# Performance work log

Measured on AMD Instinct MI355X. Metric: run time of the kernel, lower is better.

## Reference

```python
import jax, jax.numpy as jnp
import numpy as np

N = 50000
E = 800000
IN, H, OUT = 128, 96, 64
BN_EPS = 1e-5


def setup_inputs() -> dict:
    key = jax.random.key(0)
    ks = jax.random.split(key, 16)
    x = jax.random.normal(ks[0], (N, IN), dtype=jnp.float32)
    edge_index = jax.random.randint(ks[1], (2, E), 0, N, dtype=jnp.int64)
    edge_weight = jax.random.uniform(ks[2], (E,), dtype=jnp.float32)
    def lin(k, fo, fi):
        # PyG glorot-ish init
        s = 1.0 / np.sqrt(fi)
        return jax.random.uniform(k, (fo, fi), minval=-s, maxval=s, dtype=jnp.float32)
    W1, b1 = lin(ks[3], H, IN), jnp.zeros((H,), jnp.float32)
    W2, b2 = lin(ks[4], H, H), jnp.zeros((H,), jnp.float32)
    W3, b3 = lin(ks[5], OUT, H), jnp.zeros((OUT,), jnp.float32)
    g1 = jnp.ones((H,), jnp.float32); beta1 = jnp.zeros((H,), jnp.float32)
    m1 = 0.1 * jax.random.normal(ks[6], (H,), dtype=jnp.float32)
    v1 = jnp.abs(1.0 + 0.1 * jax.random.normal(ks[7], (H,), dtype=jnp.float32))
    g2 = jnp.ones((H,), jnp.float32); beta2 = jnp.zeros((H,), jnp.float32)
    m2 = 0.1 * jax.random.normal(ks[8], (H,), dtype=jnp.float32)
    v2 = jnp.abs(1.0 + 0.1 * jax.random.normal(ks[9], (H,), dtype=jnp.float32))
    return dict(x=x, edge_index=edge_index, edge_weight=edge_weight,
                W1=W1, b1=b1, W2=W2, b2=b2, W3=W3, b3=b3,
                g1=g1, beta1=beta1, m1=m1, v1=v1,
                g2=g2, beta2=beta2, m2=m2, v2=v2)


def gcn_norm(edge_index, edge_weight, n):
    # PyG gcn_norm with add_self_loops=True, fill_value=1.0
    loop = jnp.arange(n, dtype=edge_index.dtype)
    row = jnp.concatenate([edge_index[0], loop])  # sources
    col = jnp.concatenate([edge_index[1], loop])  # targets
    ew = jnp.concatenate([edge_weight, jnp.ones((n,), edge_weight.dtype)])
    deg = jax.ops.segment_sum(ew, col, num_segments=n)
    dis = jnp.where(deg > 0, jax.lax.rsqrt(deg), 0.0)  # inf -> 0 masked_fill
    norm = dis[row] * ew * dis[col]
    return row, col, norm


def gcn_conv(x, row, col, norm, W, b, n):
    xw = x @ W.T                       # [N, F_out] dense transform first
    msg = norm[:, None] * xw[row]      # [E+N, F_out] gather + edge scale
    out = jax.ops.segment_sum(msg, col, num_segments=n)  # scatter-add
    return out + b


def bn_eval(x, gamma, beta, mean, var):
    return (x - mean) * jax.lax.rsqrt(var + BN_EPS) * gamma + beta


def reference(x, edge_index, edge_weight, W1, b1, W2, b2, W3, b3,
              g1, beta1, m1, v1, g2, beta2, m2, v2):
    n = x.shape[0]
    row, col, norm = gcn_norm(edge_index, edge_weight, n)  # cached=True: shared
    h = gcn_conv(x, row, col, norm, W1, b1, n)
    h = jax.nn.relu(bn_eval(h, g1, beta1, m1, v1))
    h = gcn_conv(h, row, col, norm, W2, b2, n)
    h = jax.nn.relu(bn_eval(h, g2, beta2, m2, v2))
    out = gcn_conv(h, row, col, norm, W3, b3, n)
    return out
```

## Files before the change

### kernel.cpp

```cpp
#include <hip/hip_runtime.h>
#include <hip/hip_fp16.h>


constexpr float BN_EPS = 1e-5f;
constexpr float FIXED_SCALE = 33554432.0f;
constexpr float INV_FIXED_SCALE = 1.0f / 33554432.0f;
constexpr float NORM_SCALE = 32768.0f;
constexpr float INV_NORM_SCALE = 1.0f / 32768.0f;

typedef _Float16 f16x8 __attribute__((ext_vector_type(8)));
typedef float f32x4 __attribute__((ext_vector_type(4)));


template <int K, int F, bool F32X, bool F32W>
__device__ __forceinline__ void gemm_block(const void* __restrict__ Xin,
                                           const void* __restrict__ Win,
                                           _Float16* __restrict__ Y,
                                           int n0b, int tid, int n,
                                           _Float16* lds) {
    constexpr int KT = K / 32;
    constexpr int FT = F / 16;
    constexpr int LROW = (F == 96) ? 104 : 72;
    int wave = tid >> 6;
    int lane = tid & 63;
    int quad = lane >> 4;
    int r = lane & 15;
    int n0 = n0b + wave * 16;
    bool active = (n0 < n);

    if (active) {
        f16x8 a[KT];
        if (F32X) {
            const float* xr = (const float*)Xin + (size_t)(n0 + r) * K + quad * 8;
#pragma unroll
            for (int kt = 0; kt < KT; ++kt) {
                float4 v0 = *(const float4*)(xr + kt * 32);
                float4 v1 = *(const float4*)(xr + kt * 32 + 4);
                f16x8 t = {(_Float16)v0.x, (_Float16)v0.y, (_Float16)v0.z, (_Float16)v0.w,
                           (_Float16)v1.x, (_Float16)v1.y, (_Float16)v1.z, (_Float16)v1.w};
                a[kt] = t;
            }
        } else {
            const f16x8* xr = (const f16x8*)((const _Float16*)Xin + (size_t)(n0 + r) * K + quad * 8);
#pragma unroll
            for (int kt = 0; kt < KT; ++kt) a[kt] = xr[kt * 4];
        }

        f32x4 acc[FT];
#pragma unroll
        for (int ft = 0; ft < FT; ++ft) acc[ft] = (f32x4){0.f, 0.f, 0.f, 0.f};

#pragma unroll
        for (int kt = 0; kt < KT; ++kt) {
#pragma unroll
            for (int ft = 0; ft < FT; ++ft) {
                f16x8 b;
                if (F32W) {
                    const float* wr = (const float*)Win + (size_t)(ft * 16 + r) * K + kt * 32 + quad * 8;
                    float4 v0 = *(const float4*)wr;
                    float4 v1 = *(const float4*)(wr + 4);
                    f16x8 t = {(_Float16)v0.x, (_Float16)v0.y, (_Float16)v0.z, (_Float16)v0.w,
                               (_Float16)v1.x, (_Float16)v1.y, (_Float16)v1.z, (_Float16)v1.w};
                    b = t;
                } else {
                    b = *(const f16x8*)((const _Float16*)Win + (size_t)(ft * 16 + r) * K + kt * 32 + quad * 8);
                }
                acc[ft] = __builtin_amdgcn_mfma_f32_16x16x32_f16(a[kt], b, acc[ft], 0, 0, 0);
            }
        }

#pragma unroll
        for (int ft = 0; ft < FT; ++ft) {
#pragma unroll
            for (int reg = 0; reg < 4; ++reg) {
                int lr = wave * 16 + quad * 4 + reg;
                lds[(size_t)lr * LROW + ft * 16 + r] = (_Float16)acc[ft][reg];
            }
        }
    }
    __syncthreads();

    constexpr int CPR = F / 8;
    constexpr int TOTAL = 64 * CPR;
    for (int i = tid; i < TOTAL; i += 256) {
        int row = i / CPR, c = i - row * CPR;
        int grow = n0b + row;
        if (grow < n)
            *(uint4*)(Y + (size_t)grow * F + c * 8) =
                *(const uint4*)(lds + (size_t)row * LROW + c * 8);
    }
}

template <int K, int F>
__global__ __launch_bounds__(256) void k_gemm(const _Float16* __restrict__ X,
                                              const _Float16* __restrict__ Wh,
                                              _Float16* __restrict__ Y, int n) {
    __shared__ _Float16 lds[64 * 104];
    gemm_block<K, F, false, false>(X, Wh, Y, blockIdx.x * 64, threadIdx.x, n, lds);
}


__global__ __launch_bounds__(256) void k_mega(
    const int* __restrict__ col_idx, const float* __restrict__ ew,
    unsigned long long* packed, int* rank, int e_cnt, int pair_b,
    const float* __restrict__ x, const float* __restrict__ W1,
    _Float16* __restrict__ bufA, int n,
    const float* __restrict__ W2, const float* __restrict__ W3,
    _Float16* __restrict__ w2h, _Float16* __restrict__ w3h,
    int w2n4, int w3n4) {
    __shared__ _Float16 lds[64 * 104];
    int b = blockIdx.x;
    if (b < 2 * pair_b) {
        int q = b >> 1;
        if ((b & 1) == 0) {
#pragma unroll
            for (int j = 0; j < 4; ++j) {
                int e = q * 1024 + j * 256 + (int)threadIdx.x;
                if (e < e_cnt) {
                    int c = col_idx[e];
                    unsigned wfix = (unsigned)(ew[e] * FIXED_SCALE + 0.5f);
                    unsigned long long inc = (1ull << 32) | (unsigned long long)wfix;
                    unsigned long long old = atomicAdd(&packed[c], inc);
                    rank[e] = (int)(old >> 32);
                }
            }
        } else {
            gemm_block<128, 96, true, true>(x, W1, bufA, q * 64, threadIdx.x, n, lds);
        }
    } else {
        int i = (b - 2 * pair_b) * 256 + (int)threadIdx.x;
        const float* src; _Float16* dst; int o;
        if (i < w2n4) { src = W2; dst = w2h; o = i; }
        else if (i < w2n4 + w3n4) { src = W3; dst = w3h; o = i - w2n4; }
        else return;
        float4 v = ((const float4*)src)[o];
        __half2 h0 = __floats2half2_rn(v.x, v.y);
        __half2 h1 = __floats2half2_rn(v.z, v.w);
        *(uint2*)(dst + (size_t)o * 4) = make_uint2(*(unsigned*)&h0, *(unsigned*)&h1);
    }
}


__global__ void k_scan1(const unsigned long long* __restrict__ packed,
                        int* bsum, float* dis, int n) {
    __shared__ int s[256];
    int i = blockIdx.x * 256 + threadIdx.x;
    int cnt = 0;
    if (i < n) {
        unsigned long long p = packed[i];
        cnt = (int)(p >> 32);
        float wsum = (float)(unsigned)(p & 0xffffffffull) * INV_FIXED_SCALE;
        dis[i] = rsqrtf(1.0f + wsum);
    }
    s[threadIdx.x] = cnt;
    __syncthreads();
    for (int off = 128; off > 0; off >>= 1) {
        if ((int)threadIdx.x < off) s[threadIdx.x] += s[threadIdx.x + off];
        __syncthreads();
    }
    if (threadIdx.x == 0) bsum[blockIdx.x] = s[0];
}

__global__ void k_scan23(const unsigned long long* __restrict__ packed,
                         const int* __restrict__ bsum,
                         int* row_ptr, int n, int e_total, int nb) {
    __shared__ int sb[256];
    __shared__ int s[256];
    int t = threadIdx.x;
    int bv = (t < nb) ? bsum[t] : 0;
    sb[t] = bv;
    __syncthreads();
    for (int off = 1; off < 256; off <<= 1) {
        int x = (t >= off) ? sb[t - off] : 0;
        __syncthreads();
        sb[t] += x;
        __syncthreads();
    }
    int boff = (blockIdx.x == 0) ? 0 : sb[blockIdx.x - 1];

    int i = blockIdx.x * 256 + t;
    int v = (i < n) ? (int)(packed[i] >> 32) : 0;
    s[t] = v;
    __syncthreads();
    for (int off = 1; off < 256; off <<= 1) {
        int x = (t >= off) ? s[t - off] : 0;
        __syncthreads();
        s[t] += x;
        __syncthreads();
    }
    int ex = s[t] - v + boff;
    if (i < n) row_ptr[i] = ex;
    if (i == 0) row_ptr[n] = e_total;
}

__global__ void k_fill(const int* __restrict__ row_idx, const int* __restrict__ col_idx,
                       const float* __restrict__ ew, const float* __restrict__ dis,
                       const int* __restrict__ row_ptr, const int* __restrict__ rank,
                       unsigned* ep, int e_cnt) {
    int e = blockIdx.x * 256 + threadIdx.x;
    if (e < e_cnt) {
        int r = row_idx[e];
        int c = col_idx[e];
        float nm = dis[r] * ew[e] * dis[c];
        unsigned q = (unsigned)(nm * NORM_SCALE + 0.5f);
        if (q > 65535u) q = 65535u;
        ep[row_ptr[c] + rank[e]] = ((unsigned)r << 16) | q;
    }
}


__device__ inline void cvt8(uint4 u, float* f) {
    float2 t;
    t = __half22float2(*(const __half2*)&u.x); f[0] = t.x; f[1] = t.y;
    t = __half22float2(*(const __half2*)&u.y); f[2] = t.x; f[3] = t.y;
    t = __half22float2(*(const __half2*)&u.z); f[4] = t.x; f[5] = t.y;
    t = __half22float2(*(const __half2*)&u.w); f[6] = t.x; f[7] = t.y;
}

__device__ inline void h8_acc(uint4 u, float w, float acc[8]) {
    float2 a = __half22float2(*(const __half2*)&u.x);
    float2 b = __half22float2(*(const __half2*)&u.y);
    float2 c = __half22float2(*(const __half2*)&u.z);
    float2 d = __half22float2(*(const __half2*)&u.w);
    acc[0] = fmaf(w, a.x, acc[0]); acc[1] = fmaf(w, a.y, acc[1]);
    acc[2] = fmaf(w, b.x, acc[2]); acc[3] = fmaf(w, b.y, acc[3]);
    acc[4] = fmaf(w, c.x, acc[4]); acc[5] = fmaf(w, c.y, acc[5]);
    acc[6] = fmaf(w, d.x, acc[6]); acc[7] = fmaf(w, d.y, acc[7]);
}

template <int F, bool BN, bool F32OUT>
__global__ __launch_bounds__(256) void k_aggr(
    const _Float16* __restrict__ xw, const int* __restrict__ row_ptr,
    const unsigned* __restrict__ ep,
    const float* __restrict__ dis, const float* __restrict__ bias,
    const float* __restrict__ g, const float* __restrict__ beta,
    const float* __restrict__ m, const float* __restrict__ v,
    void* __restrict__ out, int n) {
    constexpr int FQ = F / 8;
    int tg = blockIdx.x * 256 + threadIdx.x;
    int node = tg / FQ;
    int q = tg - node * FQ;
    if (node >= n) return;

    const uint4* __restrict__ base = (const uint4*)xw;

    float acc[8];
    {
        float d = dis[node];
        float d2 = d * d;
        uint4 sv = base[(size_t)node * FQ + q];
        float t[8];
        cvt8(sv, t);
#pragma unroll
        for (int j = 0; j < 8; ++j) acc[j] = d2 * t[j];
    }

    int e0 = row_ptr[node], e1 = row_ptr[node + 1];
    int e = e0;
    for (; e + 4 <= e1; e += 4) {
        unsigned p0 = ep[e + 0], p1 = ep[e + 1], p2 = ep[e + 2], p3 = ep[e + 3];
        uint4 x0 = base[(size_t)(p0 >> 16) * FQ + q];
        uint4 x1 = base[(size_t)(p1 >> 16) * FQ + q];
        uint4 x2 = base[(size_t)(p2 >> 16) * FQ + q];
        uint4 x3 = base[(size_t)(p3 >> 16) * FQ + q];
        h8_acc(x0, (float)(p0 & 0xffffu) * INV_NORM_SCALE, acc);
        h8_acc(x1, (float)(p1 & 0xffffu) * INV_NORM_SCALE, acc);
        h8_acc(x2, (float)(p2 & 0xffffu) * INV_NORM_SCALE, acc);
        h8_acc(x3, (float)(p3 & 0xffffu) * INV_NORM_SCALE, acc);
    }
    for (; e < e1; ++e) {
        unsigned p = ep[e];
        uint4 xv = base[(size_t)(p >> 16) * FQ + q];
        h8_acc(xv, (float)(p & 0xffffu) * INV_NORM_SCALE, acc);
    }

    int fb = q * 8;
    const float4* bb = (const float4*)(bias + fb);
    float4 b0 = bb[0], b1 = bb[1];
    acc[0] += b0.x; acc[1] += b0.y; acc[2] += b0.z; acc[3] += b0.w;
    acc[4] += b1.x; acc[5] += b1.y; acc[6] += b1.z; acc[7] += b1.w;
    if (BN) {
#pragma unroll
        for (int j = 0; j < 8; ++j) {
            acc[j] = fmaxf((acc[j] - m[fb + j]) * rsqrtf(v[fb + j] + BN_EPS) * g[fb + j]
                           + beta[fb + j], 0.f);
        }
    }
    if (F32OUT) {
        float* op = (float*)out + (size_t)node * F + fb;
        *(float4*)(op + 0) = make_float4(acc[0], acc[1], acc[2], acc[3]);
        *(float4*)(op + 4) = make_float4(acc[4], acc[5], acc[6], acc[7]);
    } else {
        __half2 h0 = __floats2half2_rn(acc[0], acc[1]);
        __half2 h1 = __floats2half2_rn(acc[2], acc[3]);
        __half2 h2 = __floats2half2_rn(acc[4], acc[5]);
        __half2 h3 = __floats2half2_rn(acc[6], acc[7]);
        uint4 u = make_uint4(*(unsigned*)&h0, *(unsigned*)&h1,
                             *(unsigned*)&h2, *(unsigned*)&h3);
        ((uint4*)out)[(size_t)node * FQ + q] = u;
    }
}


extern "C" void kernel_launch(void* const* d_in, const int* in_sizes, int n_in,
                              void* d_out, int out_size, void* d_ws, size_t ws_size,
                              hipStream_t stream) {
    constexpr int IN = 128, H = 96, OUT = 64;

    const float* x   = (const float*)d_in[0];
    const int*   ei  = (const int*)d_in[1];
    const float* ew  = (const float*)d_in[2];
    const float* W1  = (const float*)d_in[3];
    const float* b1  = (const float*)d_in[4];
    const float* W2  = (const float*)d_in[5];
    const float* b2  = (const float*)d_in[6];
    const float* W3  = (const float*)d_in[7];
    const float* b3  = (const float*)d_in[8];
    const float* g1  = (const float*)d_in[9];
    const float* be1 = (const float*)d_in[10];
    const float* m1  = (const float*)d_in[11];
    const float* v1  = (const float*)d_in[12];
    const float* g2  = (const float*)d_in[13];
    const float* be2 = (const float*)d_in[14];
    const float* m2  = (const float*)d_in[15];
    const float* v2  = (const float*)d_in[16];

    const int N = in_sizes[0] / IN;
    const int E = in_sizes[2];
    const int* row_idx = ei;
    const int* col_idx = ei + E;

    char* ws = (char*)d_ws;
    size_t off = 0;
    auto alloc = [&](size_t bytes) -> void* {
        void* p = ws + off;
        off = (off + bytes + 255) & ~(size_t)255;
        return p;
    };
    unsigned long long* packed = (unsigned long long*)alloc((size_t)N * 8);
    float*     dis     = (float*)alloc((size_t)N * 4);
    int*       row_ptr = (int*)alloc((size_t)(N + 1) * 4);
    int*       bsum    = (int*)alloc(256 * 4);
    int*       rank    = (int*)alloc((size_t)E * 4);
    unsigned*  ep      = (unsigned*)alloc((size_t)E * 4);
    _Float16*  w2h     = (_Float16*)alloc((size_t)H * H * 2);
    _Float16*  w3h     = (_Float16*)alloc((size_t)OUT * H * 2);
    _Float16*  bufA    = (_Float16*)alloc((size_t)N * H * 2);
    _Float16*  bufB    = (_Float16*)alloc((size_t)N * H * 2);
    (void)ws_size; (void)n_in; (void)out_size;

    constexpr int W2N4 = H * H / 4, W3N4 = OUT * H / 4;
    const int NB = (N + 255) / 256;
    const int DEG1024 = (E + 1023) / 1024;
    const int GG = (N / 16 + 3) / 4;
    const int PAIR = (DEG1024 > GG) ? DEG1024 : GG;
    const int CVT_B = (W2N4 + W3N4 + 255) / 256;

    hipMemsetAsync(packed, 0, (size_t)N * 8, stream);
    k_mega<<<2 * PAIR + CVT_B, 256, 0, stream>>>(
        col_idx, ew, packed, rank, E, PAIR,
        x, W1, bufA, N, W2, W3, w2h, w3h, W2N4, W3N4);
    k_scan1<<<NB, 256, 0, stream>>>(packed, bsum, dis, N);
    k_scan23<<<NB, 256, 0, stream>>>(packed, bsum, row_ptr, N, E, NB);
    k_fill<<<(E + 255) / 256, 256, 0, stream>>>(row_idx, col_idx, ew, dis,
                                                row_ptr, rank, ep, E);

    const int GA96 = ((size_t)N * (H / 8) + 255) / 256;
    const int GA64 = ((size_t)N * (OUT / 8) + 255) / 256;

    k_aggr<H, true, false><<<GA96, 256, 0, stream>>>(
        bufA, row_ptr, ep, dis, b1, g1, be1, m1, v1, bufB, N);

    k_gemm<H, H><<<GG, 256, 0, stream>>>(bufB, w2h, bufA, N);
    k_aggr<H, true, false><<<GA96, 256, 0, stream>>>(
        bufA, row_ptr, ep, dis, b2, g2, be2, m2, v2, bufB, N);

    k_gemm<H, OUT><<<GG, 256, 0, stream>>>(bufB, w3h, bufA, N);
    k_aggr<OUT, false, true><<<GA64, 256, 0, stream>>>(
        bufA, row_ptr, ep, dis, b3, nullptr, nullptr, nullptr, nullptr, d_out, N);
}
```

Before: 264.9 us.

## Store GEMM outputs feature-sliced and map aggregation slices to XCDs for L2 locality

The GEMM epilogue now writes its output as separate feature slices: four slices of 24 halfs for width 96, two slices of 32 for width 64. The aggregation kernel picks its slice from the low bits of blockIdx. Because blocks are dispatched round-robin across XCDs, each XCD should mostly gather from one smaller slice that fits its L2, rather than from the whole feature matrix. The cost is narrower 48-byte gather segments per row and a dependence on the hardware's block-to-XCD scheduling order.

```diff
diff --git a/kernel.cpp b/kernel.cpp
--- a/kernel.cpp
+++ b/kernel.cpp
@@ -21,6 +21,8 @@
     constexpr int KT = K / 32;
     constexpr int FT = F / 16;
     constexpr int LROW = (F == 96) ? 104 : 72;
+    constexpr int CPS = (F == 96) ? 3 : 4;
+    constexpr int SHW = (F == 96) ? 24 : 32;
     int wave = tid >> 6;
     int lane = tid & 63;
     int quad = lane >> 4;
@@ -84,9 +86,10 @@
     constexpr int TOTAL = 64 * CPR;
     for (int i = tid; i < TOTAL; i += 256) {
         int row = i / CPR, c = i - row * CPR;
+        int s = c / CPS, off = c - s * CPS;
         int grow = n0b + row;
         if (grow < n)
-            *(uint4*)(Y + (size_t)grow * F + c * 8) =
+            *(uint4*)(Y + ((size_t)s * n + grow) * SHW + off * 8) =
                 *(const uint4*)(lds + (size_t)row * LROW + c * 8);
     }
 }
@@ -236,19 +239,23 @@
     const float* __restrict__ g, const float* __restrict__ beta,
     const float* __restrict__ m, const float* __restrict__ v,
     void* __restrict__ out, int n) {
-    constexpr int FQ = F / 8;
-    int tg = blockIdx.x * 256 + threadIdx.x;
-    int node = tg / FQ;
-    int q = tg - node * FQ;
+    constexpr int S   = (F == 96) ? 4 : 2;
+    constexpr int CPS = (F == 96) ? 3 : 4;
+    constexpr int SHW = (F == 96) ? 24 : 32;
+    constexpr int SH  = (F == 96) ? 2 : 1;
+    int sb = blockIdx.x & (S - 1);
+    int idx = ((int)blockIdx.x >> SH) * 256 + (int)threadIdx.x;
+    int node = idx / CPS;
+    int c = idx - node * CPS;
     if (node >= n) return;
 
-    const uint4* __restrict__ base = (const uint4*)xw;
+    const uint4* __restrict__ base = (const uint4*)(xw + (size_t)sb * n * SHW);
 
     float acc[8];
     {
         float d = dis[node];
         float d2 = d * d;
-        uint4 sv = base[(size_t)node * FQ + q];
+        uint4 sv = base[(size_t)node * CPS + c];
         float t[8];
         cvt8(sv, t);
 #pragma unroll
@@ -259,10 +266,10 @@
     int e = e0;
     for (; e + 4 <= e1; e += 4) {
         unsigned p0 = ep[e + 0], p1 = ep[e + 1], p2 = ep[e + 2], p3 = ep[e + 3];
-        uint4 x0 = base[(size_t)(p0 >> 16) * FQ + q];
-        uint4 x1 = base[(size_t)(p1 >> 16) * FQ + q];
-        uint4 x2 = base[(size_t)(p2 >> 16) * FQ + q];
-        uint4 x3 = base[(size_t)(p3 >> 16) * FQ + q];
+        uint4 x0 = base[(size_t)(p0 >> 16) * CPS + c];
+        uint4 x1 = base[(size_t)(p1 >> 16) * CPS + c];
+        uint4 x2 = base[(size_t)(p2 >> 16) * CPS + c];
+        uint4 x3 = base[(size_t)(p3 >> 16) * CPS + c];
         h8_acc(x0, (float)(p0 & 0xffffu) * INV_NORM_SCALE, acc);
         h8_acc(x1, (float)(p1 & 0xffffu) * INV_NORM_SCALE, acc);
         h8_acc(x2, (float)(p2 & 0xffffu) * INV_NORM_SCALE, acc);
@@ -270,11 +277,11 @@
     }
     for (; e < e1; ++e) {
         unsigned p = ep[e];
-        uint4 xv = base[(size_t)(p >> 16) * FQ + q];
+        uint4 xv = base[(size_t)(p >> 16) * CPS + c];
         h8_acc(xv, (float)(p & 0xffffu) * INV_NORM_SCALE, acc);
     }
 
-    int fb = q * 8;
+    int fb = sb * SHW + c * 8;
     const float4* bb = (const float4*)(bias + fb);
     float4 b0 = bb[0], b1 = bb[1];
     acc[0] += b0.x; acc[1] += b0.y; acc[2] += b0.z; acc[3] += b0.w;
@@ -297,7 +304,7 @@
         __half2 h3 = __floats2half2_rn(acc[6], acc[7]);
         uint4 u = make_uint4(*(unsigned*)&h0, *(unsigned*)&h1,
                              *(unsigned*)&h2, *(unsigned*)&h3);
-        ((uint4*)out)[(size_t)node * FQ + q] = u;
+        *(uint4*)((_Float16*)out + (size_t)node * F + fb) = u;
     }
 }
 
@@ -365,8 +372,8 @@
     k_fill<<<(E + 255) / 256, 256, 0, stream>>>(row_idx, col_idx, ew, dis,
                                                 row_ptr, rank, ep, E);
 
-    const int GA96 = ((size_t)N * (H / 8) + 255) / 256;
-    const int GA64 = ((size_t)N * (OUT / 8) + 255) / 256;
+    const int GA96 = 4 * ((N * 3 + 255) / 256);
+    const int GA64 = 2 * ((N * 4 + 255) / 256);
 
     k_aggr<H, true, false><<<GA96, 256, 0, stream>>>(
         bufA, row_ptr, ep, dis, b1, g1, be1, m1, v1, bufB, N);
```

New measurement: 274.9 us. 1.04x slower.
